# Performance work log

Measured on AMD Instinct MI355X. Metric: run time of the kernel, lower is better.

Reference implementation:

```python
import jax, jax.numpy as jnp
import numpy as np

# Dims: M=batch, T=time frames, B=bottleneck channels, H=intermediate channels, KK=kernel size
M, T, B, H, KK = 8, 4000, 128, 512, 3
DILATION = 2
EPS = 1e-8  # gLN eps (ConvTasNet convention)


def prelu(x, a):
    return jnp.where(x >= 0, x, a * x)


def gln(x, gamma, beta):
    # global layer norm over (time, channel) per sample; x: [M, T, C]
    m = jnp.mean(x, axis=(1, 2), keepdims=True)
    v = jnp.mean((x - m) ** 2, axis=(1, 2), keepdims=True)
    return gamma * (x - m) / jnp.sqrt(v + EPS) + beta


def depthwise_conv_same_reflect(x, w):
    # x: [M, C, L], w: [C, K]; dilation 1, 'same' padding with reflect mode
    K = w.shape[1]
    pl = (K - 1) // 2
    xp = jnp.pad(x, ((0, 0), (0, 0), (pl, K - 1 - pl)), mode='reflect')
    return jax.lax.conv_general_dilated(
        xp, w[:, None, :], (1,), 'VALID',
        feature_group_count=x.shape[1], dimension_numbers=('NCH', 'OIH', 'NCH'))


def setup_inputs() -> dict:
    key = jax.random.key(0)
    ks = jax.random.split(key, 12)
    f32 = jnp.float32
    return {
        'x': jax.random.normal(ks[0], (M, T, B), f32),
        'conv1_w': jax.random.normal(ks[1], (H, B), f32) * 0.05,
        'prelu1_a': jnp.asarray(0.25, f32),
        'norm1_g': jnp.ones((H,), f32),
        'norm1_b': jnp.zeros((H,), f32),
        'off_dw_w': jax.random.normal(ks[2], (H, KK), f32) * 0.02,
        'odc_prelu_a': jnp.asarray(0.25, f32),
        'off_pw_w': jax.random.normal(ks[3], (KK, H), f32) * 0.02,
        'opc_prelu_a': jnp.asarray(0.25, f32),
        'dw_w': jax.random.normal(ks[4], (H, KK), f32) * 0.05,
        'dw_b': jax.random.normal(ks[5], (H,), f32) * 0.01,
        'prelu2_a': jnp.asarray(0.25, f32),
        'norm2_g': jnp.ones((H,), f32),
        'norm2_b': jnp.zeros((H,), f32),
        'pw_w': jax.random.normal(ks[6], (B, H), f32) * 0.05,
    }


def reference(x, conv1_w, prelu1_a, norm1_g, norm1_b,
              off_dw_w, odc_prelu_a, off_pw_w, opc_prelu_a,
              dw_w, dw_b, prelu2_a, norm2_g, norm2_b, pw_w):
    dtype = x.dtype
    residual = x
    # 1x1 bottleneck conv -> PReLU -> gLN
    h = jnp.einsum('mtb,hb->mth', x, conv1_w)
    h = gln(prelu(h, prelu1_a), norm1_g, norm1_b)
    hc = jnp.moveaxis(h, 1, 2)  # [M, H, T]

    # --- offset prediction branch (PackedDeformConv1d) ---
    off = depthwise_conv_same_reflect(hc, off_dw_w)          # [M, H, T]
    off = prelu(off, odc_prelu_a)
    off = jnp.einsum('mct,kc->mkt', off, off_pw_w)           # [M, KK, T]
    off = prelu(off, opc_prelu_a)
    offsets = jnp.moveaxis(off, 1, 2)                        # [M, T, KK]

    # --- deformable depthwise conv (same padding, reflect) ---
    pad_tot = DILATION * (KK - 1)
    pl = pad_tot // 2
    xp = jnp.pad(hc, ((0, 0), (0, 0), (pl, pad_tot - pl)), mode='reflect')  # [M,H,Lp]
    Lp = T + pad_tot
    dil_pos = (jnp.arange(KK) * DILATION).astype(dtype)      # [KK]: 0, d, 2d
    t0 = jnp.arange(T, dtype=dtype)[:, None]                 # [T,1]
    Tpos = t0 + dil_pos[None, :] + offsets                   # [M,T,KK]
    Tpos = jnp.clip(Tpos, t0, t0 + dil_pos[-1])              # constrain to receptive field
    U = jnp.clip(jnp.floor(Tpos).astype(jnp.int32), 0, Lp - 2)
    Uf = U.astype(dtype)
    g0 = jax.nn.relu(1.0 - jnp.abs(Uf - Tpos))               # [M,T,KK]
    g1 = jax.nn.relu(1.0 - jnp.abs(Uf + 1.0 - Tpos))
    idx = jnp.broadcast_to(U.reshape(M, 1, T * KK), (M, H, T * KK))
    s0 = jnp.take_along_axis(xp, idx, axis=2).reshape(M, H, T, KK)
    s1 = jnp.take_along_axis(xp, idx + 1, axis=2).reshape(M, H, T, KK)
    sampled = g0[:, None] * s0 + g1[:, None] * s1            # [M,H,T,KK]
    y = jnp.einsum('mhtk,hk->mht', sampled, dw_w) + dw_b[None, :, None]

    # PReLU -> gLN -> 1x1 conv back to B channels, residual add
    y = jnp.moveaxis(y, 1, 2)                                # [M,T,H]
    y = gln(prelu(y, prelu2_a), norm2_g, norm2_b)
    out = jnp.einsum('mth,bh->mtb', y, pw_w)
    return out + residual
```

## Files before the change

### kernel.cpp

```cpp
#include <hip/hip_runtime.h>

#define Mdim 8
#define Tdim 4000
#define Bdim 128
#define Hdim 512
#define NPER (Tdim*Hdim)
#define EPSG 1e-8f

typedef __attribute__((ext_vector_type(8))) short short8;
typedef __attribute__((ext_vector_type(4))) float floatx4;

static __device__ __forceinline__ float bits2f(unsigned short s) {
  union { unsigned int u; float f; } v; v.u = ((unsigned int)s) << 16; return v.f;
}
static __device__ __forceinline__ unsigned short f2bits(float f) {
  union { float f; unsigned int u; } v; v.f = f;
  unsigned int u = v.u;
  u += 0x7fffu + ((u >> 16) & 1u);
  return (unsigned short)(u >> 16);
}
static __device__ __forceinline__ short8 pack8(const float4& a, const float4& b) {
  short8 v;
  v[0]=(short)f2bits(a.x); v[1]=(short)f2bits(a.y); v[2]=(short)f2bits(a.z); v[3]=(short)f2bits(a.w);
  v[4]=(short)f2bits(b.x); v[5]=(short)f2bits(b.y); v[6]=(short)f2bits(b.z); v[7]=(short)f2bits(b.w);
  return v;
}

__global__ __launch_bounds__(256) void k_conv1(
    const float* __restrict__ x,
    const float* __restrict__ w1,
    const float* __restrict__ a1p,
    unsigned short* __restrict__ Hbuf,
    float2* __restrict__ part1)
{
  __shared__ __align__(16) unsigned short ldsW[64*136];
  __shared__ __align__(16) unsigned short ltile[64*72];
  __shared__ float red[512];

  const int tid = threadIdx.x;
  const int t0 = blockIdx.x * 64;
  const int hh = blockIdx.y;
  const int m  = blockIdx.z;

  const int lane = tid & 63, wv = tid >> 6, quad = lane >> 4, l16 = lane & 15;
  int tr = t0 + wv*16 + l16;
  int trc = tr < Tdim ? tr : Tdim-1;
  const float* xrow = x + ((size_t)m*Tdim + trc)*Bdim;
  short8 afr[4];
  #pragma unroll
  for (int ks = 0; ks < 4; ++ks) {
    float4 fa = *(const float4*)&xrow[ks*32 + quad*8];
    float4 fb = *(const float4*)&xrow[ks*32 + quad*8 + 4];
    afr[ks] = pack8(fa, fb);
  }

  const float a1 = a1p[0];
  float lsum = 0.f, lss = 0.f;

  for (int hc = 0; hc < 4; ++hc) {
    const int h0 = (hh*4 + hc) * 64;
    __syncthreads();
    #pragma unroll
    for (int it = 0; it < 4; ++it) {
      int idx = (it*256 + tid) * 8;
      int r = idx >> 7, c = idx & 127;
      float4 fa = *(const float4*)&w1[(size_t)(h0 + r)*Bdim + c];
      float4 fb = *(const float4*)&w1[(size_t)(h0 + r)*Bdim + c + 4];
      *(short8*)&ldsW[r*136 + c] = pack8(fa, fb);
    }
    __syncthreads();

    floatx4 acc[4] = {};
    #pragma unroll
    for (int ks = 0; ks < 4; ++ks) {
      #pragma unroll
      for (int nt = 0; nt < 4; ++nt) {
        short8 bfr = *(const short8*)&ldsW[(nt*16 + l16)*136 + ks*32 + quad*8];
        acc[nt] = __builtin_amdgcn_mfma_f32_16x16x32_bf16(afr[ks], bfr, acc[nt], 0, 0, 0);
      }
    }

    #pragma unroll
    for (int nt = 0; nt < 4; ++nt) {
      int hl = nt*16 + l16;
      #pragma unroll
      for (int r = 0; r < 4; ++r) {
        int tl = wv*16 + quad*4 + r;
        float v = acc[nt][r];
        v = v >= 0.f ? v : a1 * v;
        if (t0 + tl < Tdim) { lsum += v; lss += v*v; }
        ltile[tl*72 + hl] = f2bits(v);
      }
    }
    __syncthreads();
    {
      int tr2 = tid >> 2, ck = (tid & 3) * 16;
      int tg = t0 + tr2;
      if (tg < Tdim) {
        unsigned short* dst = &Hbuf[((size_t)m*Tdim + tg)*Hdim + h0 + ck];
        *(short8*)&dst[0] = *(const short8*)&ltile[tr2*72 + ck];
        *(short8*)&dst[8] = *(const short8*)&ltile[tr2*72 + ck + 8];
      }
    }
  }

  red[tid] = lsum; red[256 + tid] = lss;
  __syncthreads();
  for (int s = 128; s > 0; s >>= 1) {
    if (tid < s) { red[tid] += red[tid + s]; red[256+tid] += red[256+tid+s]; }
    __syncthreads();
  }
  if (tid == 0)
    part1[((size_t)m*2 + hh)*63 + blockIdx.x] = make_float2(red[0], red[256]);
}

__global__ __launch_bounds__(256) void k_deform(
    const unsigned short* __restrict__ Hbuf,
    const float2* __restrict__ part1,
    const float* __restrict__ g1w,
    const float* __restrict__ b1w,
    const float* __restrict__ odw,
    const float* __restrict__ aodcp,
    const float* __restrict__ opw,
    const float* __restrict__ aopcp,
    const float* __restrict__ dww,
    const float* __restrict__ dwb,
    const float* __restrict__ a2p,
    unsigned short* __restrict__ Ybuf,
    float2* __restrict__ part2)
{
  __shared__ float s_stats[2];
  __shared__ float rsum[4], rss[4];
  const int tid = threadIdx.x, lane = tid & 63, w = tid >> 6;
  const int tb = blockIdx.x*8 + w*2;
  const int m = blockIdx.y;
  const int c8 = lane*8;
  const unsigned short* base = Hbuf + (size_t)m*Tdim*Hdim;

  short8 hrow[2][3];
  #pragma unroll
  for (int tt = 0; tt < 2; ++tt) {
    int t = tb + tt;
    int tm1 = (t == 0) ? 1 : t-1;
    int tp1 = (t == Tdim-1) ? Tdim-2 : t+1;
    hrow[tt][0] = *(const short8*)&base[(size_t)tm1*Hdim + c8];
    hrow[tt][1] = *(const short8*)&base[(size_t)t  *Hdim + c8];
    hrow[tt][2] = *(const short8*)&base[(size_t)tp1*Hdim + c8];
  }
  float g1v[8], b1v[8];
  #pragma unroll
  for (int j = 0; j < 8; j += 4) {
    *(float4*)&g1v[j] = *(const float4*)&g1w[c8 + j];
    *(float4*)&b1v[j] = *(const float4*)&b1w[c8 + j];
  }

  if (tid < 64) {
    float s = 0.f, q = 0.f;
    for (int i = lane; i < 126; i += 64) {
      float2 p = part1[(size_t)m*126 + i];
      s += p.x; q += p.y;
    }
    #pragma unroll
    for (int st = 32; st > 0; st >>= 1) { s += __shfl_xor(s, st); q += __shfl_xor(q, st); }
    if (lane == 0) { s_stats[0] = s; s_stats[1] = q; }
  }
  __syncthreads();
  const float invn = 1.0f/(float)NPER;
  const float mean1 = s_stats[0]*invn;
  const float var1  = fmaxf(s_stats[1]*invn - mean1*mean1, 0.f);
  const float inv1  = 1.0f/sqrtf(var1 + EPSG);

  float oa[2][3] = {};
  {
    const float aodc = aodcp[0];
    float wod[24], q0v[8], q1v[8], q2v[8];
    #pragma unroll
    for (int j = 0; j < 8; j += 4) {
      *(float4*)&q0v[j] = *(const float4*)&opw[c8 + j];
      *(float4*)&q1v[j] = *(const float4*)&opw[Hdim + c8 + j];
      *(float4*)&q2v[j] = *(const float4*)&opw[2*Hdim + c8 + j];
    }
    #pragma unroll
    for (int j = 0; j < 24; j += 4)
      *(float4*)&wod[j] = *(const float4*)&odw[c8*3 + j];

    #pragma unroll
    for (int j = 0; j < 8; ++j) {
      float A = g1v[j] * inv1;
      float C = b1v[j] - mean1*A;
      #pragma unroll
      for (int tt = 0; tt < 2; ++tt) {
        float fm = fmaf(A, bits2f((unsigned short)hrow[tt][0][j]), C);
        float fz = fmaf(A, bits2f((unsigned short)hrow[tt][1][j]), C);
        float fp = fmaf(A, bits2f((unsigned short)hrow[tt][2][j]), C);
        float d = fm*wod[j*3+0] + fz*wod[j*3+1] + fp*wod[j*3+2];
        d = d >= 0.f ? d : aodc*d;
        oa[tt][0] = fmaf(d, q0v[j], oa[tt][0]);
        oa[tt][1] = fmaf(d, q1v[j], oa[tt][1]);
        oa[tt][2] = fmaf(d, q2v[j], oa[tt][2]);
      }
    }
    #pragma unroll
    for (int s = 32; s > 0; s >>= 1) {
      #pragma unroll
      for (int tt = 0; tt < 2; ++tt) {
        oa[tt][0] += __shfl_xor(oa[tt][0], s);
        oa[tt][1] += __shfl_xor(oa[tt][1], s);
        oa[tt][2] += __shfl_xor(oa[tt][2], s);
      }
    }
  }

  const float aopc = aopcp[0];
  const float a2   = a2p[0];
  int I0[2][3], I1[2][3]; float G0[2][3], G1[2][3], GS[2][3];
  #pragma unroll
  for (int tt = 0; tt < 2; ++tt) {
    const float tf = (float)(tb + tt);
    #pragma unroll
    for (int k = 0; k < 3; ++k) {
      float off = oa[tt][k];
      off = off >= 0.f ? off : aopc*off;
      float pos = tf + (float)(2*k) + off;
      pos = fminf(fmaxf(pos, tf), tf + 4.0f);
      int U = (int)floorf(pos);
      if (U > Tdim + 2) U = Tdim + 2;
      float Uf = (float)U;
      G0[tt][k] = fmaxf(0.f, 1.f - fabsf(Uf - pos));
      G1[tt][k] = fmaxf(0.f, 1.f - fabsf(Uf + 1.f - pos));
      GS[tt][k] = G0[tt][k] + G1[tt][k];
      int ia = U - 2; ia = ia < 0 ? -ia : ia; if (ia > Tdim-1) ia = 2*(Tdim-1) - ia;
      int ib = U - 1; ib = ib < 0 ? -ib : ib; if (ib > Tdim-1) ib = 2*(Tdim-1) - ib;
      I0[tt][k] = ia; I1[tt][k] = ib;
    }
  }

  short8 s0v[2][3], s1v[2][3];
  #pragma unroll
  for (int tt = 0; tt < 2; ++tt)
    #pragma unroll
    for (int k = 0; k < 3; ++k) {
      s0v[tt][k] = *(const short8*)&base[(size_t)I0[tt][k]*Hdim + c8];
      s1v[tt][k] = *(const short8*)&base[(size_t)I1[tt][k]*Hdim + c8];
    }

  float bv[8], wd[24];
  #pragma unroll
  for (int j = 0; j < 8; j += 4)
    *(float4*)&bv[j] = *(const float4*)&dwb[c8 + j];
  #pragma unroll
  for (int j = 0; j < 24; j += 4)
    *(float4*)&wd[j] = *(const float4*)&dww[c8*3 + j];

  float lsum = 0.f, lss = 0.f;
  short8 yv[2];
  #pragma unroll
  for (int j = 0; j < 8; ++j) {
    float A = g1v[j] * inv1;
    float C = b1v[j] - mean1*A;
    float w0 = wd[j*3+0], w1 = wd[j*3+1], w2 = wd[j*3+2];
    #pragma unroll
    for (int tt = 0; tt < 2; ++tt) {
      float ybase = fmaf(C, w0*GS[tt][0] + w1*GS[tt][1] + w2*GS[tt][2], bv[j]);
      float t0s = fmaf(G1[tt][0], bits2f((unsigned short)s1v[tt][0][j]), G0[tt][0]*bits2f((unsigned short)s0v[tt][0][j]));
      float t1s = fmaf(G1[tt][1], bits2f((unsigned short)s1v[tt][1][j]), G0[tt][1]*bits2f((unsigned short)s0v[tt][1][j]));
      float t2s = fmaf(G1[tt][2], bits2f((unsigned short)s1v[tt][2][j]), G0[tt][2]*bits2f((unsigned short)s0v[tt][2][j]));
      float acc = w0*t0s + w1*t1s + w2*t2s;
      float y = fmaf(A, acc, ybase);
      float p = y >= 0.f ? y : a2*y;
      lsum += p; lss += p*p;
      yv[tt][j] = (short)f2bits(p);
    }
  }
  #pragma unroll
  for (int tt = 0; tt < 2; ++tt)
    *(short8*)&Ybuf[((size_t)m*Tdim + tb + tt)*Hdim + c8] = yv[tt];

  #pragma unroll
  for (int s = 32; s > 0; s >>= 1) {
    lsum += __shfl_xor(lsum, s);
    lss  += __shfl_xor(lss, s);
  }
  if (lane == 0) { rsum[w] = lsum; rss[w] = lss; }
  __syncthreads();
  if (tid == 0)
    part2[(size_t)m*500 + blockIdx.x] =
      make_float2(rsum[0]+rsum[1]+rsum[2]+rsum[3], rss[0]+rss[1]+rss[2]+rss[3]);
}

__global__ __launch_bounds__(64) void k_w2(
    const float2* __restrict__ part2,
    const float* __restrict__ g2w,
    const float* __restrict__ b2w,
    const float* __restrict__ pww,
    unsigned short* __restrict__ W2,
    float* __restrict__ const2)
{
  const int bid = blockIdx.x;
  const int m = bid >> 7, b = bid & 127;
  const int tid = threadIdx.x;

  float s = 0.f, q = 0.f;
  for (int i = tid; i < 500; i += 64) {
    float2 p = part2[(size_t)m*500 + i];
    s += p.x; q += p.y;
  }
  #pragma unroll
  for (int st = 32; st > 0; st >>= 1) { s += __shfl_xor(s, st); q += __shfl_xor(q, st); }

  const float invn = 1.0f/(float)NPER;
  const float mean2 = s*invn;
  const float var2  = fmaxf(q*invn - mean2*mean2, 0.f);
  const float inv2  = 1.0f/sqrtf(var2 + EPSG);

  const int j8 = tid*8;
  float g2v[8], b2v[8], pv[8];
  #pragma unroll
  for (int j = 0; j < 8; j += 4) {
    *(float4*)&g2v[j] = *(const float4*)&g2w[j8 + j];
    *(float4*)&b2v[j] = *(const float4*)&b2w[j8 + j];
    *(float4*)&pv[j]  = *(const float4*)&pww[(size_t)b*Hdim + j8 + j];
  }
  float csum = 0.f;
  short8 wv8;
  #pragma unroll
  for (int j = 0; j < 8; ++j) {
    float A = g2v[j] * inv2;
    float C = b2v[j] - mean2*A;
    csum = fmaf(C, pv[j], csum);
    wv8[j] = (short)f2bits(A*pv[j]);
  }
  *(short8*)&W2[((size_t)m*Bdim + b)*Hdim + j8] = wv8;

  #pragma unroll
  for (int st = 32; st > 0; st >>= 1) csum += __shfl_down(csum, st);
  if (tid == 0) const2[m*Bdim + b] = csum;
}

__global__ __launch_bounds__(256) void k_out(
    const unsigned short* __restrict__ Ybuf,
    const unsigned short* __restrict__ W2,
    const float* __restrict__ const2,
    const float* __restrict__ x,
    float* __restrict__ out)
{
  __shared__ __align__(16) unsigned short ldsW[64*136];
  __shared__ __align__(16) float ltf[64*68];
  const int tid = threadIdx.x;
  const int t0 = blockIdx.x*64;
  const int n0 = blockIdx.y*64;
  const int m  = blockIdx.z;
  const int lane = tid & 63, wv = tid >> 6, quad = lane >> 4, l16 = lane & 15;
  int tr = t0 + wv*16 + l16;
  int trc = tr < Tdim ? tr : Tdim-1;
  const unsigned short* arow = Ybuf + ((size_t)m*Tdim + trc)*Hdim;
  floatx4 acc[4] = {};
  for (int kc = 0; kc < 4; ++kc) {
    __syncthreads();
    #pragma unroll
    for (int it = 0; it < 4; ++it) {
      int idx = (it*256 + tid)*8;
      int r = idx >> 7, c = idx & 127;
      *(short8*)&ldsW[r*136 + c] =
        *(const short8*)&W2[((size_t)m*Bdim + n0 + r)*Hdim + kc*128 + c];
    }
    __syncthreads();
    #pragma unroll
    for (int ks = 0; ks < 4; ++ks) {
      short8 afr = *(const short8*)&arow[kc*128 + ks*32 + quad*8];
      #pragma unroll
      for (int nt = 0; nt < 4; ++nt) {
        short8 bfr = *(const short8*)&ldsW[(nt*16 + l16)*136 + ks*32 + quad*8];
        acc[nt] = __builtin_amdgcn_mfma_f32_16x16x32_bf16(afr, bfr, acc[nt], 0, 0, 0);
      }
    }
  }
  __syncthreads();
  #pragma unroll
  for (int nt = 0; nt < 4; ++nt) {
    int bl = nt*16 + l16;
    float cb = const2[m*Bdim + n0 + bl];
    #pragma unroll
    for (int r = 0; r < 4; ++r) {
      int tl = wv*16 + quad*4 + r;
      ltf[tl*68 + bl] = acc[nt][r] + cb;
    }
  }
  __syncthreads();
  {
    int tr2 = tid >> 2, ck = (tid & 3) * 16;
    int tg = t0 + tr2;
    if (tg < Tdim) {
      const float* xr = &x[((size_t)m*Tdim + tg)*Bdim + n0 + ck];
      float* orow = &out[((size_t)m*Tdim + tg)*Bdim + n0 + ck];
      #pragma unroll
      for (int j = 0; j < 4; ++j) {
        float4 v = *(const float4*)&ltf[tr2*68 + ck + j*4];
        float4 rx = *(const float4*)&xr[j*4];
        v.x += rx.x; v.y += rx.y; v.z += rx.z; v.w += rx.w;
        *(float4*)&orow[j*4] = v;
      }
    }
  }
}

extern "C" void kernel_launch(void* const* d_in, const int* in_sizes, int n_in,
                              void* d_out, int out_size, void* d_ws, size_t ws_size,
                              hipStream_t stream)
{
  (void)in_sizes; (void)n_in; (void)out_size; (void)ws_size;
  const float* x    = (const float*)d_in[0];
  const float* w1   = (const float*)d_in[1];
  const float* a1   = (const float*)d_in[2];
  const float* g1   = (const float*)d_in[3];
  const float* b1   = (const float*)d_in[4];
  const float* odw  = (const float*)d_in[5];
  const float* aodc = (const float*)d_in[6];
  const float* opw  = (const float*)d_in[7];
  const float* aopc = (const float*)d_in[8];
  const float* dww  = (const float*)d_in[9];
  const float* dwb  = (const float*)d_in[10];
  const float* a2   = (const float*)d_in[11];
  const float* g2   = (const float*)d_in[12];
  const float* b2   = (const float*)d_in[13];
  const float* pww  = (const float*)d_in[14];
  float* out = (float*)d_out;

  char* ws = (char*)d_ws;
  const size_t OFF_P1 = 0;
  const size_t OFF_C2 = 8192;
  const size_t OFF_P2 = 12288;
  const size_t OFF_W2 = 44288;
  const size_t OFF_H  = 1092864;
  const size_t OFF_Y  = 33860864;
  float2* part1  = (float2*)(ws + OFF_P1);
  float*  const2 = (float*)(ws + OFF_C2);
  float2* part2  = (float2*)(ws + OFF_P2);
  unsigned short* W2   = (unsigned short*)(ws + OFF_W2);
  unsigned short* Hbuf = (unsigned short*)(ws + OFF_H);
  unsigned short* Ybuf = (unsigned short*)(ws + OFF_Y);

  k_conv1 <<<dim3(63, 2, 8), 256, 0, stream>>>(x, w1, a1, Hbuf, part1);
  k_deform<<<dim3(500, 8), 256, 0, stream>>>(Hbuf, part1, g1, b1, odw, aodc, opw, aopc, dww, dwb, a2, Ybuf, part2);
  k_w2    <<<dim3(1024), 64, 0, stream>>>(part2, g2, b2, pww, W2, const2);
  k_out   <<<dim3(63, 2, 8), 256, 0, stream>>>(Ybuf, W2, const2, x, out);
}
```

Baseline: 165.6 us.

## Pre-swizzle weights into MFMA fragment layout and fold gLN2 stats into output GEMM

A new prep kernel converts conv1 and the output pointwise weights to bf16 once, laid out in MFMA B-fragment order. The GEMM kernels can then load fragments straight from global memory instead of staging weights through LDS behind block-wide barriers. The k_w2 kernel is removed: the gLN2 statistics are reduced inside k_out and applied as a per-row scale plus bias correction, which lets the weights stay independent of the sample. k_conv1 is also re-tiled to 32-row blocks where each wave covers half of H, with wave-local LDS fences replacing __syncthreads. The trade is redundant stat reduction in every output block and uncached global fragment loads.

```diff
diff --git a/kernel.cpp b/kernel.cpp
--- a/kernel.cpp
+++ b/kernel.cpp
@@ -26,26 +26,82 @@
   return v;
 }
 
+#define LDS_FENCE() do { \
+  asm volatile("s_waitcnt lgkmcnt(0)" ::: "memory"); \
+  __builtin_amdgcn_sched_barrier(0); \
+} while (0)
+
+__global__ __launch_bounds__(256) void k_prep(
+    const float* __restrict__ w1,
+    const float* __restrict__ pww,
+    const float* __restrict__ g2w,
+    const float* __restrict__ b2w,
+    unsigned short* __restrict__ w1r,
+    unsigned short* __restrict__ W2g,
+    float* __restrict__ Sv,
+    float* __restrict__ B2s)
+{
+  const int tid = threadIdx.x;
+  if (blockIdx.x < 32) {
+    int i = blockIdx.x*256 + tid;
+    int lane = i & 63, f = i >> 6;
+    int nt = f & 3, ks = (f >> 2) & 3, hc = f >> 4;
+    int h = hc*64 + nt*16 + (lane & 15);
+    int c = ks*32 + (lane >> 4)*8;
+    const float* src = &w1[(size_t)h*Bdim + c];
+    float4 a = *(const float4*)src;
+    float4 b = *(const float4*)(src + 4);
+    *(short8*)&w1r[(size_t)i*8] = pack8(a, b);
+  } else {
+    const int b = (blockIdx.x - 32)*4 + (tid >> 6);
+    const int sub = tid & 63;
+    const int j8 = sub*8;
+    float pv[8], g2v[8], b2v[8];
+    #pragma unroll
+    for (int j = 0; j < 8; j += 4) {
+      *(float4*)&pv[j]  = *(const float4*)&pww[(size_t)b*Hdim + j8 + j];
+      *(float4*)&g2v[j] = *(const float4*)&g2w[j8 + j];
+      *(float4*)&b2v[j] = *(const float4*)&b2w[j8 + j];
+    }
+    float sS = 0.f, sB = 0.f;
+    short8 wv8;
+    #pragma unroll
+    for (int j = 0; j < 8; ++j) {
+      float pg = pv[j]*g2v[j];
+      sS += pg;
+      sB += pv[j]*b2v[j];
+      wv8[j] = (short)f2bits(pg);
+    }
+    {
+      int half = b >> 6, nt = (b >> 4) & 3, l16 = b & 15;
+      int kc = sub >> 4, ks = (sub >> 2) & 3, quad = sub & 3;
+      int lane = quad*16 + l16;
+      size_t f = (((size_t)(half*4 + kc)*4 + ks)*4 + nt);
+      *(short8*)&W2g[(f*64 + lane)*8] = wv8;
+    }
+    #pragma unroll
+    for (int st = 32; st > 0; st >>= 1) { sS += __shfl_xor(sS, st); sB += __shfl_xor(sB, st); }
+    if (sub == 0) { Sv[b] = sS; B2s[b] = sB; }
+  }
+}
+
 __global__ __launch_bounds__(256) void k_conv1(
     const float* __restrict__ x,
-    const float* __restrict__ w1,
+    const unsigned short* __restrict__ w1r,
     const float* __restrict__ a1p,
     unsigned short* __restrict__ Hbuf,
     float2* __restrict__ part1)
 {
-  __shared__ __align__(16) unsigned short ldsW[64*136];
-  __shared__ __align__(16) unsigned short ltile[64*72];
+  __shared__ __align__(16) unsigned short ltile[4][16*72];
   __shared__ float red[512];
 
   const int tid = threadIdx.x;
-  const int t0 = blockIdx.x * 64;
-  const int hh = blockIdx.y;
-  const int m  = blockIdx.z;
-
-  const int lane = tid & 63, wv = tid >> 6, quad = lane >> 4, l16 = lane & 15;
-  int tr = t0 + wv*16 + l16;
-  int trc = tr < Tdim ? tr : Tdim-1;
-  const float* xrow = x + ((size_t)m*Tdim + trc)*Bdim;
+  const int t0 = blockIdx.x * 32;
+  const int m  = blockIdx.y;
+  const int lane = tid & 63, w = tid >> 6, quad = lane >> 4, l16 = lane & 15;
+  const int tsub = w & 1, hh = w >> 1;
+  const int tbase = t0 + tsub*16;
+  const float* xrow = x + ((size_t)m*Tdim + tbase + l16)*Bdim;
   short8 afr[4];
   #pragma unroll
   for (int ks = 0; ks < 4; ++ks) {
@@ -55,53 +111,40 @@
   }
 
   const float a1 = a1p[0];
+  const short8* wf = (const short8*)w1r + lane;
   float lsum = 0.f, lss = 0.f;
 
-  for (int hc = 0; hc < 4; ++hc) {
-    const int h0 = (hh*4 + hc) * 64;
-    __syncthreads();
-    #pragma unroll
-    for (int it = 0; it < 4; ++it) {
-      int idx = (it*256 + tid) * 8;
-      int r = idx >> 7, c = idx & 127;
-      float4 fa = *(const float4*)&w1[(size_t)(h0 + r)*Bdim + c];
-      float4 fb = *(const float4*)&w1[(size_t)(h0 + r)*Bdim + c + 4];
-      *(short8*)&ldsW[r*136 + c] = pack8(fa, fb);
-    }
-    __syncthreads();
-
+  #pragma unroll
+  for (int hc4 = 0; hc4 < 4; ++hc4) {
+    const int hcg = hh*4 + hc4;
     floatx4 acc[4] = {};
     #pragma unroll
-    for (int ks = 0; ks < 4; ++ks) {
-      #pragma unroll
-      for (int nt = 0; nt < 4; ++nt) {
-        short8 bfr = *(const short8*)&ldsW[(nt*16 + l16)*136 + ks*32 + quad*8];
-        acc[nt] = __builtin_amdgcn_mfma_f32_16x16x32_bf16(afr[ks], bfr, acc[nt], 0, 0, 0);
-      }
-    }
+    for (int ks = 0; ks < 4; ++ks)
+      #pragma unroll
+      for (int nt = 0; nt < 4; ++nt)
+        acc[nt] = __builtin_amdgcn_mfma_f32_16x16x32_bf16(
+            afr[ks], wf[(hcg*16 + ks*4 + nt)*64], acc[nt], 0, 0, 0);
 
     #pragma unroll
     for (int nt = 0; nt < 4; ++nt) {
       int hl = nt*16 + l16;
       #pragma unroll
       for (int r = 0; r < 4; ++r) {
-        int tl = wv*16 + quad*4 + r;
+        int tl = quad*4 + r;
         float v = acc[nt][r];
         v = v >= 0.f ? v : a1 * v;
-        if (t0 + tl < Tdim) { lsum += v; lss += v*v; }
-        ltile[tl*72 + hl] = f2bits(v);
+        lsum += v; lss += v*v;
+        ltile[w][tl*72 + hl] = f2bits(v);
       }
     }
-    __syncthreads();
+    LDS_FENCE();
     {
-      int tr2 = tid >> 2, ck = (tid & 3) * 16;
-      int tg = t0 + tr2;
-      if (tg < Tdim) {
-        unsigned short* dst = &Hbuf[((size_t)m*Tdim + tg)*Hdim + h0 + ck];
-        *(short8*)&dst[0] = *(const short8*)&ltile[tr2*72 + ck];
-        *(short8*)&dst[8] = *(const short8*)&ltile[tr2*72 + ck + 8];
-      }
-    }
+      int row = lane >> 2, ck = (lane & 3) * 16;
+      unsigned short* dst = &Hbuf[((size_t)m*Tdim + tbase + row)*Hdim + hcg*64 + ck];
+      *(short8*)&dst[0] = *(const short8*)&ltile[w][row*72 + ck];
+      *(short8*)&dst[8] = *(const short8*)&ltile[w][row*72 + ck + 8];
+    }
+    LDS_FENCE();
   }
 
   red[tid] = lsum; red[256 + tid] = lss;
@@ -111,7 +154,7 @@
     __syncthreads();
   }
   if (tid == 0)
-    part1[((size_t)m*2 + hh)*63 + blockIdx.x] = make_float2(red[0], red[256]);
+    part1[(size_t)m*125 + blockIdx.x] = make_float2(red[0], red[256]);
 }
 
 __global__ __launch_bounds__(256) void k_deform(
@@ -156,8 +199,8 @@
 
   if (tid < 64) {
     float s = 0.f, q = 0.f;
-    for (int i = lane; i < 126; i += 64) {
-      float2 p = part1[(size_t)m*126 + i];
+    for (int i = lane; i < 125; i += 64) {
+      float2 p = part1[(size_t)m*125 + i];
       s += p.x; q += p.y;
     }
     #pragma unroll
@@ -288,105 +331,72 @@
       make_float2(rsum[0]+rsum[1]+rsum[2]+rsum[3], rss[0]+rss[1]+rss[2]+rss[3]);
 }
 
-__global__ __launch_bounds__(64) void k_w2(
-    const float2* __restrict__ part2,
-    const float* __restrict__ g2w,
-    const float* __restrict__ b2w,
-    const float* __restrict__ pww,
-    unsigned short* __restrict__ W2,
-    float* __restrict__ const2)
-{
-  const int bid = blockIdx.x;
-  const int m = bid >> 7, b = bid & 127;
-  const int tid = threadIdx.x;
-
-  float s = 0.f, q = 0.f;
-  for (int i = tid; i < 500; i += 64) {
-    float2 p = part2[(size_t)m*500 + i];
-    s += p.x; q += p.y;
-  }
-  #pragma unroll
-  for (int st = 32; st > 0; st >>= 1) { s += __shfl_xor(s, st); q += __shfl_xor(q, st); }
-
-  const float invn = 1.0f/(float)NPER;
-  const float mean2 = s*invn;
-  const float var2  = fmaxf(q*invn - mean2*mean2, 0.f);
-  const float inv2  = 1.0f/sqrtf(var2 + EPSG);
-
-  const int j8 = tid*8;
-  float g2v[8], b2v[8], pv[8];
-  #pragma unroll
-  for (int j = 0; j < 8; j += 4) {
-    *(float4*)&g2v[j] = *(const float4*)&g2w[j8 + j];
-    *(float4*)&b2v[j] = *(const float4*)&b2w[j8 + j];
-    *(float4*)&pv[j]  = *(const float4*)&pww[(size_t)b*Hdim + j8 + j];
-  }
-  float csum = 0.f;
-  short8 wv8;
-  #pragma unroll
-  for (int j = 0; j < 8; ++j) {
-    float A = g2v[j] * inv2;
-    float C = b2v[j] - mean2*A;
-    csum = fmaf(C, pv[j], csum);
-    wv8[j] = (short)f2bits(A*pv[j]);
-  }
-  *(short8*)&W2[((size_t)m*Bdim + b)*Hdim + j8] = wv8;
-
-  #pragma unroll
-  for (int st = 32; st > 0; st >>= 1) csum += __shfl_down(csum, st);
-  if (tid == 0) const2[m*Bdim + b] = csum;
-}
-
 __global__ __launch_bounds__(256) void k_out(
     const unsigned short* __restrict__ Ybuf,
-    const unsigned short* __restrict__ W2,
-    const float* __restrict__ const2,
+    const unsigned short* __restrict__ W2g,
+    const float2* __restrict__ part2,
+    const float* __restrict__ Sv,
+    const float* __restrict__ B2s,
     const float* __restrict__ x,
     float* __restrict__ out)
 {
-  __shared__ __align__(16) unsigned short ldsW[64*136];
   __shared__ __align__(16) float ltf[64*68];
+  __shared__ float rsA[4], rsB[4];
   const int tid = threadIdx.x;
   const int t0 = blockIdx.x*64;
-  const int n0 = blockIdx.y*64;
+  const int half = blockIdx.y;
+  const int n0 = half*64;
   const int m  = blockIdx.z;
   const int lane = tid & 63, wv = tid >> 6, quad = lane >> 4, l16 = lane & 15;
+
+  {
+    float s = 0.f, q = 0.f;
+    for (int i = tid; i < 500; i += 256) {
+      float2 p = part2[(size_t)m*500 + i];
+      s += p.x; q += p.y;
+    }
+    #pragma unroll
+    for (int st = 32; st > 0; st >>= 1) { s += __shfl_xor(s, st); q += __shfl_xor(q, st); }
+    if (lane == 0) { rsA[wv] = s; rsB[wv] = q; }
+  }
+
   int tr = t0 + wv*16 + l16;
   int trc = tr < Tdim ? tr : Tdim-1;
   const unsigned short* arow = Ybuf + ((size_t)m*Tdim + trc)*Hdim;
+  const short8* wf = (const short8*)W2g + (size_t)half*64*64 + lane;
+
   floatx4 acc[4] = {};
-  for (int kc = 0; kc < 4; ++kc) {
-    __syncthreads();
-    #pragma unroll
-    for (int it = 0; it < 4; ++it) {
-      int idx = (it*256 + tid)*8;
-      int r = idx >> 7, c = idx & 127;
-      *(short8*)&ldsW[r*136 + c] =
-        *(const short8*)&W2[((size_t)m*Bdim + n0 + r)*Hdim + kc*128 + c];
-    }
-    __syncthreads();
+  #pragma unroll
+  for (int kc = 0; kc < 4; ++kc)
     #pragma unroll
     for (int ks = 0; ks < 4; ++ks) {
       short8 afr = *(const short8*)&arow[kc*128 + ks*32 + quad*8];
       #pragma unroll
-      for (int nt = 0; nt < 4; ++nt) {
-        short8 bfr = *(const short8*)&ldsW[(nt*16 + l16)*136 + ks*32 + quad*8];
-        acc[nt] = __builtin_amdgcn_mfma_f32_16x16x32_bf16(afr, bfr, acc[nt], 0, 0, 0);
-      }
-    }
-  }
+      for (int nt = 0; nt < 4; ++nt)
+        acc[nt] = __builtin_amdgcn_mfma_f32_16x16x32_bf16(
+            afr, wf[((kc*4 + ks)*4 + nt)*64], acc[nt], 0, 0, 0);
+    }
+
   __syncthreads();
+  const float Ssum = rsA[0]+rsA[1]+rsA[2]+rsA[3];
+  const float Qsum = rsB[0]+rsB[1]+rsB[2]+rsB[3];
+  const float invn = 1.0f/(float)NPER;
+  const float mean2 = Ssum*invn;
+  const float var2  = fmaxf(Qsum*invn - mean2*mean2, 0.f);
+  const float inv2  = 1.0f/sqrtf(var2 + EPSG);
+  const float ms2   = inv2*mean2;
+
   #pragma unroll
   for (int nt = 0; nt < 4; ++nt) {
     int bl = nt*16 + l16;
-    float cb = const2[m*Bdim + n0 + bl];
+    float cb = B2s[n0 + bl] - ms2*Sv[n0 + bl];
     #pragma unroll
     for (int r = 0; r < 4; ++r) {
       int tl = wv*16 + quad*4 + r;
-      ltf[tl*68 + bl] = acc[nt][r] + cb;
-    }
-  }
-  __syncthreads();
+      ltf[tl*68 + bl] = fmaf(inv2, acc[nt][r], cb);
+    }
+  }
+  LDS_FENCE();
   {
     int tr2 = tid >> 2, ck = (tid & 3) * 16;
     int tg = t0 + tr2;
@@ -427,21 +437,25 @@
   float* out = (float*)d_out;
 
   char* ws = (char*)d_ws;
-  const size_t OFF_P1 = 0;
-  const size_t OFF_C2 = 8192;
-  const size_t OFF_P2 = 12288;
-  const size_t OFF_W2 = 44288;
-  const size_t OFF_H  = 1092864;
-  const size_t OFF_Y  = 33860864;
-  float2* part1  = (float2*)(ws + OFF_P1);
-  float*  const2 = (float*)(ws + OFF_C2);
-  float2* part2  = (float2*)(ws + OFF_P2);
-  unsigned short* W2   = (unsigned short*)(ws + OFF_W2);
+  const size_t OFF_P1  = 0;
+  const size_t OFF_P2  = 8192;
+  const size_t OFF_S   = 40960;
+  const size_t OFF_B2S = 41472;
+  const size_t OFF_W1R = 45056;
+  const size_t OFF_W2G = 176128;
+  const size_t OFF_H   = 307200;
+  const size_t OFF_Y   = 33075200;
+  float2* part1 = (float2*)(ws + OFF_P1);
+  float2* part2 = (float2*)(ws + OFF_P2);
+  float*  Sv    = (float*)(ws + OFF_S);
+  float*  B2s   = (float*)(ws + OFF_B2S);
+  unsigned short* w1r  = (unsigned short*)(ws + OFF_W1R);
+  unsigned short* W2g  = (unsigned short*)(ws + OFF_W2G);
   unsigned short* Hbuf = (unsigned short*)(ws + OFF_H);
   unsigned short* Ybuf = (unsigned short*)(ws + OFF_Y);
 
-  k_conv1 <<<dim3(63, 2, 8), 256, 0, stream>>>(x, w1, a1, Hbuf, part1);
+  k_prep  <<<dim3(64), 256, 0, stream>>>(w1, pww, g2, b2, w1r, W2g, Sv, B2s);
+  k_conv1 <<<dim3(125, 8), 256, 0, stream>>>(x, w1r, a1, Hbuf, part1);
   k_deform<<<dim3(500, 8), 256, 0, stream>>>(Hbuf, part1, g1, b1, odw, aodc, opw, aopc, dww, dwb, a2, Ybuf, part2);
-  k_w2    <<<dim3(1024), 64, 0, stream>>>(part2, g2, b2, pww, W2, const2);
-  k_out   <<<dim3(63, 2, 8), 256, 0, stream>>>(Ybuf, W2, const2, x, out);
-}
+  k_out   <<<dim3(63, 2, 8), 256, 0, stream>>>(Ybuf, W2g, part2, Sv, B2s, x, out);
+}
```

After: 166.2 us. About the same (+0.4%).
